# Kernel optimization log

Hardware: AMD Instinct MI355X
Metric: run time of the kernel (lower is better)

Reference implementation:

```python
import jax, jax.numpy as jnp
import numpy as np

KSIZE = 7
SIGMA = 3.0
ALPHA = 0.1
POS_VAL_FOR_ALL_NEG = 5.0
NEG_VAL_FOR_ALL_POS = -5.0


def _gauss_kernel():
    x = jnp.arange(KSIZE, dtype=jnp.float32) - (KSIZE - 1) / 2.0
    pdf = jnp.exp(-0.5 * (x / SIGMA) ** 2)
    return pdf / pdf.sum()


def _gaussian_blur(img):
    # img: (B, C, H, W); separable 7x7 gaussian, reflect padding (torchvision behavior)
    B, C, H, W = img.shape
    k = _gauss_kernel()
    pad = KSIZE // 2
    x = jnp.pad(img, ((0, 0), (0, 0), (pad, pad), (pad, pad)), mode='reflect')
    x = x.reshape(B * C, 1, H + 2 * pad, W + 2 * pad)
    kh = k.reshape(1, 1, KSIZE, 1)
    kw = k.reshape(1, 1, 1, KSIZE)
    x = jax.lax.conv_general_dilated(x, kh, (1, 1), 'VALID')
    x = jax.lax.conv_general_dilated(x, kw, (1, 1), 'VALID')
    return x.reshape(B, C, H, W)


def _dup_map(x, mask, fallback):
    # x, mask: (L,). Gather x[mask] (original order) then tile to length L.
    # Stable argsort puts True(=selected) positions first in original order.
    L = x.shape[0]
    cnt = mask.sum()
    order = jnp.argsort(jnp.logical_not(mask))  # selected indices first, stable
    idx = order[jnp.arange(L) % jnp.maximum(cnt, 1)]
    return jnp.where(cnt == 0, jnp.float32(fallback), x[idx])


_dup_vmapped = jax.vmap(_dup_map, in_axes=(0, 0, None))


def _bce_with_logits(x, y):
    # mean( max(x,0) - x*y + log1p(exp(-|x|)) ) == mean( softplus(x) - x*y )
    return jnp.mean(jnp.logaddexp(0.0, x) - x * y)


def _forward(inp, tgt):
    B, C, H, W = inp.shape
    aug_sim_target = (_gaussian_blur(tgt * 255.0) > 0).astype(jnp.float32)

    L = H * W
    x = inp.reshape(B * C, L)
    t = tgt.reshape(B * C, L)
    a = aug_sim_target.reshape(B * C, L)

    # duplicated_pos: gather input at target>0, tile; fallback +5 if no positives
    pos_mask = t > 0
    dup_pos = _dup_vmapped(x, pos_mask, POS_VAL_FOR_ALL_NEG)

    # duplicated_false_pos: prefer (input>0 & ~aug_pos); else all negatives; else -5
    aug_pos = a > 0
    fp_mask = jnp.logical_and(x > 0, jnp.logical_not(aug_pos))
    neg_mask = jnp.logical_not(aug_pos)
    cnt_fp = fp_mask.sum(axis=1, keepdims=True)
    chosen_mask = jnp.where(cnt_fp > 0, fp_mask, neg_mask)
    dup_fp = _dup_vmapped(x, chosen_mask, NEG_VAL_FOR_ALL_POS)

    sim = dup_pos * x
    aug_sim = dup_pos * dup_fp

    sim_loss = _bce_with_logits(sim, t) + _bce_with_logits(dup_pos, jnp.ones_like(x))
    aug_sim_loss = _bce_with_logits(aug_sim, jnp.zeros_like(x))
    return sim_loss + ALPHA * aug_sim_loss


def setup_inputs() -> dict:
    key = jax.random.key(0)
    k1, k2 = jax.random.split(key)
    B, C, H, W = 16, 3, 512, 512
    inp = jax.random.normal(k1, (B, C, H, W), dtype=jnp.float32)
    tgt = jax.random.randint(k2, (B, C, H, W), 0, 2).astype(jnp.float32)
    return {"input": inp, "target": tgt}


def reference(input, target):
    return _forward(input, target)
```

## Files before the change

### kernel.cpp

```cpp
#include <hip/hip_runtime.h>
#include <math.h>

constexpr int W = 512;
constexpr int HIMG = 512;
constexpr int L = 1 << 18;
constexpr int LOG2L = 18;
constexpr int TPB = 256;
constexpr int TILE = 2048;
constexpr int TILES_PER_ROW = L / TILE;
constexpr int WORDS_PER_ROW = L / 64;
constexpr int WORDS_PER_TILE = TILE / 64;
constexpr int LBLK = 32;
constexpr int CHUNK = L / LBLK;
constexpr int LIT = CHUNK / (TPB * 4);

typedef unsigned long long ull;

__device__ __forceinline__ float softplus_f(float v) {
    return fmaxf(v, 0.0f) +
           0.6931471805599453f *
               __builtin_amdgcn_logf(1.0f + __builtin_amdgcn_exp2f(-fabsf(v) * 1.4426950408889634f));
}

__device__ __forceinline__ ull hdil7(ull prev, ull cur, ull next) {
    ull r = cur;
    r |= (cur >> 1) | (next << 63);
    r |= (cur >> 2) | (next << 62);
    r |= (cur >> 3) | (next << 61);
    r |= (cur << 1) | (prev >> 63);
    r |= (cur << 2) | (prev >> 62);
    r |= (cur << 3) | (prev >> 61);
    return r;
}

template <typename T>
__device__ __forceinline__ T sel8(const T* a, int k) {
    return k == 0 ? a[0] : k == 1 ? a[1] : k == 2 ? a[2] : k == 3 ? a[3]
         : k == 4 ? a[4] : k == 5 ? a[5] : k == 6 ? a[6] : a[7];
}

__global__ void mask_dilh_kernel(const float* __restrict__ x, const float* __restrict__ t,
                                 ull* __restrict__ maskT, ull* __restrict__ maskX,
                                 ull* __restrict__ maskH, float* __restrict__ out,
                                 int nScan) {
    if (blockIdx.x == 0 && threadIdx.x == 0) out[0] = 0.0f;
    int lane = threadIdx.x & 63;
    int wave = (blockIdx.x * TPB + threadIdx.x) >> 6;
    int nW = (gridDim.x * TPB) >> 6;
    for (int s = wave; s < nScan; s += nW) {
        int eb = s << 9;
        ull wt[8], wx[8], h[8];
#pragma unroll
        for (int k = 0; k < 8; ++k) {
            wt[k] = __ballot(t[eb + k * 64 + lane] > 0.0f);
            wx[k] = __ballot(x[eb + k * 64 + lane] > 0.0f);
        }
#pragma unroll
        for (int k = 0; k < 8; ++k) {
            ull cur = wt[k];
            ull prev = k ? wt[k - 1]
                         : ((((cur >> 1) & 1ull) << 63) | (((cur >> 2) & 1ull) << 62) |
                            (((cur >> 3) & 1ull) << 61));
            ull next = (k < 7) ? wt[k + 1]
                               : (((cur >> 62) & 1ull) | (((cur >> 61) & 1ull) << 1) |
                                  (((cur >> 60) & 1ull) << 2));
            h[k] = hdil7(prev, cur, next);
        }
        int w0 = s << 3;
        int k = lane & 7;
        if (lane < 8) maskT[w0 + k] = sel8(wt, k);
        else if (lane < 16) maskX[w0 + k] = sel8(wx, k);
        else if (lane < 24) maskH[w0 + k] = sel8(h, k);
    }
}

__global__ __launch_bounds__(TPB)
void dilv_count_kernel(const ull* __restrict__ maskT, const ull* __restrict__ maskX,
                       const ull* __restrict__ maskH, ull* __restrict__ maskA,
                       int* __restrict__ oPos, int* __restrict__ oCh,
                       int* __restrict__ rCp, int* __restrict__ rCc,
                       ull* __restrict__ rMp, ull* __restrict__ rMc,
                       int* __restrict__ rUseFp) {
    int r = blockIdx.x;
    int tid = threadIdx.x;
    __shared__ ull sh[WORDS_PER_ROW];
    __shared__ unsigned char pw[WORDS_PER_ROW], fw[WORDS_PER_ROW], nw[WORDS_PER_ROW];
    int base = r * WORDS_PER_ROW;
#pragma unroll
    for (int c = 0; c < WORDS_PER_ROW / TPB; ++c) {
        int w = c * TPB + tid;
        sh[w] = maskH[base + w];
    }
    __syncthreads();
#pragma unroll
    for (int c = 0; c < WORDS_PER_ROW / TPB; ++c) {
        int w = c * TPB + tid;
        int scan = w >> 3, col = w & 7;
        ull wa = 0;
#pragma unroll
        for (int d = -3; d <= 3; ++d) {
            int ii = scan + d;
            ii = ii < 0 ? -ii : (ii > HIMG - 1 ? 2 * (HIMG - 1) - ii : ii);
            wa |= sh[ii * 8 + col];
        }
        maskA[base + w] = wa;
        ull wt = maskT[base + w], wx = maskX[base + w];
        pw[w] = (unsigned char)__popcll(wt);
        fw[w] = (unsigned char)__popcll(wx & ~wa);
        nw[w] = (unsigned char)(64 - __popcll(wa));
    }
    __syncthreads();
    __shared__ int ssp[TILES_PER_ROW], ssf[TILES_PER_ROW], ssn[TILES_PER_ROW];
    int myp = 0, myf = 0, myn = 0;
    if (tid < TILES_PER_ROW) {
        int wb = tid * WORDS_PER_TILE;
#pragma unroll 8
        for (int k = 0; k < WORDS_PER_TILE; ++k) {
            myp += pw[wb + k]; myf += fw[wb + k]; myn += nw[wb + k];
        }
        ssp[tid] = myp; ssf[tid] = myf; ssn[tid] = myn;
    }
    __syncthreads();
    for (int off = 1; off < TILES_PER_ROW; off <<= 1) {
        int ap = 0, af = 0, an = 0;
        bool act = (tid < TILES_PER_ROW && tid >= off);
        if (act) { ap = ssp[tid - off]; af = ssf[tid - off]; an = ssn[tid - off]; }
        __syncthreads();
        if (act) { ssp[tid] += ap; ssf[tid] += af; ssn[tid] += an; }
        __syncthreads();
    }
    if (tid < TILES_PER_ROW) {
        int cp = ssp[TILES_PER_ROW - 1], cf = ssf[TILES_PER_ROW - 1], cn = ssn[TILES_PER_ROW - 1];
        bool useFp = cf > 0;
        int tile = r * TILES_PER_ROW + tid;
        oPos[tile] = ssp[tid] - myp;
        oCh[tile] = useFp ? (ssf[tid] - myf) : (ssn[tid] - myn);
        if (tid == 0) {
            int cc = useFp ? cf : cn;
            rCp[r] = cp; rCc[r] = cc; rUseFp[r] = useFp ? 1 : 0;
            ull dp_ = (ull)(cp > 0 ? cp : 1);
            ull dc_ = (ull)(cc > 0 ? cc : 1);
            rMp[r] = ((1ull << 40) + dp_ - 1) / dp_;
            rMc[r] = ((1ull << 40) + dc_ - 1) / dc_;
        }
    }
}

__global__ void scatter_kernel(const float* __restrict__ x,
                               const ull* __restrict__ maskT, const ull* __restrict__ maskX,
                               const ull* __restrict__ maskA,
                               const int* __restrict__ oPos, const int* __restrict__ oCh,
                               const int* __restrict__ rUseFp,
                               float* __restrict__ xp, float* __restrict__ xf) {
    int tile = blockIdx.x;
    int tid = threadIdx.x;
    int r = tile >> 7;
    bool useFp = rUseFp[r] != 0;
    int widx = tile * WORDS_PER_TILE + (tid >> 3);
    int shift = (tid & 7) * 8;
    ull wa = maskA[widx];
    unsigned bT = (unsigned)(maskT[widx] >> shift) & 0xFF;
    unsigned bCh = useFp ? ((unsigned)((maskX[widx] & ~wa) >> shift) & 0xFF)
                         : ((unsigned)((~wa) >> shift) & 0xFF);
    const float4* x4 = (const float4*)x;
    int b4 = tile * (TILE / 4) + tid * 2;
    float4 a = x4[b4], b = x4[b4 + 1];
    float xv[8] = {a.x, a.y, a.z, a.w, b.x, b.y, b.z, b.w};
    int p = __popc(bT), c = __popc(bCh);
    __shared__ int s[TPB];
    int v = p | (c << 16);
    s[tid] = v;
    __syncthreads();
    for (int off = 1; off < TPB; off <<= 1) {
        int add = tid >= off ? s[tid - off] : 0;
        __syncthreads();
        s[tid] += add;
        __syncthreads();
    }
    int excl = s[tid] - v;
    int rL = r << LOG2L;
    int pwi = rL + oPos[tile] + (excl & 0xFFFF);
    int cwi = rL + oCh[tile] + (excl >> 16);
#pragma unroll
    for (int e = 0; e < 8; ++e) {
        if ((bT >> e) & 1) xp[pwi++] = xv[e];
        if ((bCh >> e) & 1) xf[cwi++] = xv[e];
    }
}

__global__ __launch_bounds__(TPB)
void loss_kernel(const float* __restrict__ x, const ull* __restrict__ maskT,
                 const float* __restrict__ xp, const float* __restrict__ xf,
                 const int* __restrict__ rCp, const int* __restrict__ rCc,
                 const ull* __restrict__ rMp, const ull* __restrict__ rMc,
                 float* __restrict__ out, double inv_ntot) {
    int r = blockIdx.x >> 5;
    int cb = (blockIdx.x & 31) * CHUNK;
    int rL = r << LOG2L;
    int cp = rCp[r], cc = rCc[r];
    ull Mp = rMp[r], Mc = rMc[r];
    const float4* x4 = (const float4*)(x + rL + cb);
    const float* xpr = xp + rL;
    const float* xfr = xf + rL;
    const ull* mtr = maskT + (rL >> 6);
    float local = 0.0f;
#pragma unroll
    for (int it = 0; it < LIT; ++it) {
        int o4 = it * TPB + threadIdx.x;
        unsigned l = (unsigned)(cb + (o4 << 2));
        float4 xv = x4[o4];
        unsigned tb = (unsigned)(mtr[l >> 6] >> (l & 63)) & 0xFu;
        float dps[4], dfs[4];
        if (cp > 0) {
            unsigned d = (unsigned)cp;
            unsigned q = (unsigned)(((ull)l * Mp) >> 40);
            unsigned m0 = l - q * d;
            unsigned m1 = m0 + 1; if (m1 == d) m1 = 0;
            unsigned m2 = m1 + 1; if (m2 == d) m2 = 0;
            unsigned m3 = m2 + 1; if (m3 == d) m3 = 0;
            dps[0] = xpr[m0]; dps[1] = xpr[m1]; dps[2] = xpr[m2]; dps[3] = xpr[m3];
        } else {
            dps[0] = dps[1] = dps[2] = dps[3] = 5.0f;
        }
        if (cc > 0) {
            unsigned d = (unsigned)cc;
            unsigned q = (unsigned)(((ull)l * Mc) >> 40);
            unsigned m0 = l - q * d;
            unsigned m1 = m0 + 1; if (m1 == d) m1 = 0;
            unsigned m2 = m1 + 1; if (m2 == d) m2 = 0;
            unsigned m3 = m2 + 1; if (m3 == d) m3 = 0;
            dfs[0] = xfr[m0]; dfs[1] = xfr[m1]; dfs[2] = xfr[m2]; dfs[3] = xfr[m3];
        } else {
            dfs[0] = dfs[1] = dfs[2] = dfs[3] = -5.0f;
        }
        float xs[4] = {xv.x, xv.y, xv.z, xv.w};
#pragma unroll
        for (int k = 0; k < 4; ++k) {
            float sim = dps[k] * xs[k];
            float e = softplus_f(sim) + softplus_f(-dps[k]) + 0.1f * softplus_f(dps[k] * dfs[k]);
            if ((tb >> k) & 1) e -= sim;
            local += e;
        }
    }
    __shared__ double sd[TPB];
    int tid = threadIdx.x;
    sd[tid] = (double)local;
    __syncthreads();
    for (int off = TPB / 2; off > 0; off >>= 1) {
        if (tid < off) sd[tid] += sd[tid + off];
        __syncthreads();
    }
    if (tid == 0) atomicAdd(out, (float)(sd[0] * inv_ntot));
}

extern "C" void kernel_launch(void* const* d_in, const int* in_sizes, int n_in,
                              void* d_out, int out_size, void* d_ws, size_t ws_size,
                              hipStream_t stream) {
    const float* x = (const float*)d_in[0];
    const float* t = (const float*)d_in[1];
    float* out = (float*)d_out;

    int ntot = in_sizes[0];
    int R = ntot >> LOG2L;
    int numTiles = ntot / TILE;
    int nwords = ntot / 64;
    int nScan = ntot / W;

    char* ws = (char*)d_ws;
    size_t off = 0;
    auto alloc = [&](size_t bytes) {
        size_t p = off;
        off = (off + bytes + 255) & ~(size_t)255;
        return (void*)(ws + p);
    };
    ull* maskT = (ull*)alloc((size_t)nwords * 8);
    ull* maskX = (ull*)alloc((size_t)nwords * 8);
    ull* maskH = (ull*)alloc((size_t)nwords * 8);
    ull* maskA = (ull*)alloc((size_t)nwords * 8);
    int* oPos = (int*)alloc(numTiles * sizeof(int));
    int* oCh  = (int*)alloc(numTiles * sizeof(int));
    int* rCp = (int*)alloc(R * sizeof(int));
    int* rCc = (int*)alloc(R * sizeof(int));
    int* rUseFp = (int*)alloc(R * sizeof(int));
    ull* rMp = (ull*)alloc(R * sizeof(ull));
    ull* rMc = (ull*)alloc(R * sizeof(ull));
    float* xp = (float*)alloc((size_t)ntot * sizeof(float));
    float* xf = (float*)alloc((size_t)ntot * sizeof(float));

    mask_dilh_kernel<<<1536, TPB, 0, stream>>>(x, t, maskT, maskX, maskH, out, nScan);
    dilv_count_kernel<<<R, TPB, 0, stream>>>(maskT, maskX, maskH, maskA, oPos, oCh,
                                             rCp, rCc, rMp, rMc, rUseFp);
    scatter_kernel<<<numTiles, TPB, 0, stream>>>(x, maskT, maskX, maskA, oPos, oCh, rUseFp,
                                                 xp, xf);
    loss_kernel<<<R * LBLK, TPB, 0, stream>>>(x, maskT, xp, xf, rCp, rCc, rMp, rMc, out,
                                              1.0 / (double)ntot);
}
```

Before: 176.1 us.

## Fuse horizontal and vertical dilation with per-tile counting; coalesce scatter via LDS staging

Merges the mask/horizontal-dilation kernel and the vertical-dilation/count kernel into one kernel. Each block handles 32 scanlines plus a 3-row halo in shared memory and emits the false-positive and negative masks along with per-tile counts through wave shuffles. A small scan kernel then computes the row offsets. The scatter kernel now stages compacted values in LDS and writes them out contiguously, replacing per-thread scattered stores. The cost is recomputing the halo rows of the target ballots and extra LDS use in scatter.

```diff
diff --git a/kernel.cpp b/kernel.cpp
--- a/kernel.cpp
+++ b/kernel.cpp
@@ -8,8 +8,11 @@
 constexpr int TPB = 256;
 constexpr int TILE = 2048;
 constexpr int TILES_PER_ROW = L / TILE;
-constexpr int WORDS_PER_ROW = L / 64;
 constexpr int WORDS_PER_TILE = TILE / 64;
+constexpr int SPB = 32;
+constexpr int HALO = 3;
+constexpr int HBUF = SPB + 2 * HALO;
+constexpr int BLK_PER_IMG = HIMG / SPB;
 constexpr int LBLK = 32;
 constexpr int CHUNK = L / LBLK;
 constexpr int LIT = CHUNK / (TPB * 4);
@@ -39,21 +42,35 @@
          : k == 4 ? a[4] : k == 5 ? a[5] : k == 6 ? a[6] : a[7];
 }
 
-__global__ void mask_dilh_kernel(const float* __restrict__ x, const float* __restrict__ t,
-                                 ull* __restrict__ maskT, ull* __restrict__ maskX,
-                                 ull* __restrict__ maskH, float* __restrict__ out,
-                                 int nScan) {
+__global__ __launch_bounds__(TPB)
+void fused_mask_kernel(const float* __restrict__ x, const float* __restrict__ t,
+                       ull* __restrict__ mT, ull* __restrict__ mFp, ull* __restrict__ mNeg,
+                       int* __restrict__ cPos, int* __restrict__ cFp, int* __restrict__ cNeg,
+                       float* __restrict__ out) {
     if (blockIdx.x == 0 && threadIdx.x == 0) out[0] = 0.0f;
+    int b = blockIdx.x;
+    int img = b >> 4;
+    int y0 = (b & 15) * SPB;
+    int gs0 = img * HIMG + y0;
+
+    __shared__ ull hbuf[HBUF][8];
+    __shared__ ull tbuf[SPB][8];
+    __shared__ ull xbuf[SPB][8];
+
     int lane = threadIdx.x & 63;
-    int wave = (blockIdx.x * TPB + threadIdx.x) >> 6;
-    int nW = (gridDim.x * TPB) >> 6;
-    for (int s = wave; s < nScan; s += nW) {
-        int eb = s << 9;
+    int wv = threadIdx.x >> 6;
+    int ylo = (y0 - HALO < 0) ? 0 : y0 - HALO;
+    int yhi = (y0 + SPB - 1 + HALO > HIMG - 1) ? HIMG - 1 : y0 + SPB - 1 + HALO;
+
+    for (int yl = ylo + wv; yl <= yhi; yl += 4) {
+        int gbase = (img * HIMG + yl) * W;
+        bool own = (yl >= y0) && (yl < y0 + SPB);
         ull wt[8], wx[8], h[8];
 #pragma unroll
-        for (int k = 0; k < 8; ++k) {
-            wt[k] = __ballot(t[eb + k * 64 + lane] > 0.0f);
-            wx[k] = __ballot(x[eb + k * 64 + lane] > 0.0f);
+        for (int k = 0; k < 8; ++k) wt[k] = __ballot(t[gbase + k * 64 + lane] > 0.0f);
+        if (own) {
+#pragma unroll
+            for (int k = 0; k < 8; ++k) wx[k] = __ballot(x[gbase + k * 64 + lane] > 0.0f);
         }
 #pragma unroll
         for (int k = 0; k < 8; ++k) {
@@ -66,108 +83,107 @@
                                   (((cur >> 60) & 1ull) << 2));
             h[k] = hdil7(prev, cur, next);
         }
-        int w0 = s << 3;
+        int hy = yl - (y0 - HALO);
         int k = lane & 7;
-        if (lane < 8) maskT[w0 + k] = sel8(wt, k);
-        else if (lane < 16) maskX[w0 + k] = sel8(wx, k);
-        else if (lane < 24) maskH[w0 + k] = sel8(h, k);
-    }
-}
-
-__global__ __launch_bounds__(TPB)
-void dilv_count_kernel(const ull* __restrict__ maskT, const ull* __restrict__ maskX,
-                       const ull* __restrict__ maskH, ull* __restrict__ maskA,
-                       int* __restrict__ oPos, int* __restrict__ oCh,
-                       int* __restrict__ rCp, int* __restrict__ rCc,
-                       ull* __restrict__ rMp, ull* __restrict__ rMc,
-                       int* __restrict__ rUseFp) {
+        if (lane < 8) {
+            hbuf[hy][k] = sel8(h, k);
+        } else if (own && lane < 16) {
+            tbuf[yl - y0][k] = sel8(wt, k);
+            mT[(img * HIMG + yl) * 8 + k] = sel8(wt, k);
+        } else if (own && lane < 24) {
+            xbuf[yl - y0][k] = sel8(wx, k);
+        }
+    }
+    __syncthreads();
+
+    int tid = threadIdx.x;
+    int ys = tid >> 3;
+    int c = tid & 7;
+    int y = y0 + ys;
+    ull wa = 0;
+#pragma unroll
+    for (int d = -3; d <= 3; ++d) {
+        int yy = y + d;
+        yy = yy < 0 ? -yy : (yy > HIMG - 1 ? 2 * (HIMG - 1) - yy : yy);
+        wa |= hbuf[yy - (y0 - HALO)][c];
+    }
+    ull tw = tbuf[ys][c];
+    ull fp = xbuf[ys][c] & ~wa;
+    ull ng = ~wa;
+    int gw = gs0 * 8 + tid;
+    mFp[gw] = fp;
+    mNeg[gw] = ng;
+    int pT = __popcll(tw), pF = __popcll(fp), pN = __popcll(ng);
+#pragma unroll
+    for (int m = 1; m < 32; m <<= 1) {
+        pT += __shfl_xor(pT, m, 64);
+        pF += __shfl_xor(pF, m, 64);
+        pN += __shfl_xor(pN, m, 64);
+    }
+    if ((lane & 31) == 0) {
+        int tile = img * TILES_PER_ROW + (y0 >> 2) + (tid >> 5);
+        cPos[tile] = pT; cFp[tile] = pF; cNeg[tile] = pN;
+    }
+}
+
+__global__ void scan_kernel(const int* __restrict__ cPos, const int* __restrict__ cFp,
+                            const int* __restrict__ cNeg,
+                            int* __restrict__ oPos, int* __restrict__ oCh,
+                            int* __restrict__ rCp, int* __restrict__ rCc,
+                            ull* __restrict__ rMp, ull* __restrict__ rMc,
+                            int* __restrict__ rUseFp) {
     int r = blockIdx.x;
     int tid = threadIdx.x;
-    __shared__ ull sh[WORDS_PER_ROW];
-    __shared__ unsigned char pw[WORDS_PER_ROW], fw[WORDS_PER_ROW], nw[WORDS_PER_ROW];
-    int base = r * WORDS_PER_ROW;
-#pragma unroll
-    for (int c = 0; c < WORDS_PER_ROW / TPB; ++c) {
-        int w = c * TPB + tid;
-        sh[w] = maskH[base + w];
-    }
-    __syncthreads();
-#pragma unroll
-    for (int c = 0; c < WORDS_PER_ROW / TPB; ++c) {
-        int w = c * TPB + tid;
-        int scan = w >> 3, col = w & 7;
-        ull wa = 0;
-#pragma unroll
-        for (int d = -3; d <= 3; ++d) {
-            int ii = scan + d;
-            ii = ii < 0 ? -ii : (ii > HIMG - 1 ? 2 * (HIMG - 1) - ii : ii);
-            wa |= sh[ii * 8 + col];
-        }
-        maskA[base + w] = wa;
-        ull wt = maskT[base + w], wx = maskX[base + w];
-        pw[w] = (unsigned char)__popcll(wt);
-        fw[w] = (unsigned char)__popcll(wx & ~wa);
-        nw[w] = (unsigned char)(64 - __popcll(wa));
-    }
-    __syncthreads();
     __shared__ int ssp[TILES_PER_ROW], ssf[TILES_PER_ROW], ssn[TILES_PER_ROW];
-    int myp = 0, myf = 0, myn = 0;
-    if (tid < TILES_PER_ROW) {
-        int wb = tid * WORDS_PER_TILE;
-#pragma unroll 8
-        for (int k = 0; k < WORDS_PER_TILE; ++k) {
-            myp += pw[wb + k]; myf += fw[wb + k]; myn += nw[wb + k];
-        }
-        ssp[tid] = myp; ssf[tid] = myf; ssn[tid] = myn;
-    }
+    int myp = cPos[r * TILES_PER_ROW + tid];
+    int myf = cFp[r * TILES_PER_ROW + tid];
+    int myn = cNeg[r * TILES_PER_ROW + tid];
+    ssp[tid] = myp; ssf[tid] = myf; ssn[tid] = myn;
     __syncthreads();
     for (int off = 1; off < TILES_PER_ROW; off <<= 1) {
         int ap = 0, af = 0, an = 0;
-        bool act = (tid < TILES_PER_ROW && tid >= off);
-        if (act) { ap = ssp[tid - off]; af = ssf[tid - off]; an = ssn[tid - off]; }
-        __syncthreads();
-        if (act) { ssp[tid] += ap; ssf[tid] += af; ssn[tid] += an; }
-        __syncthreads();
-    }
-    if (tid < TILES_PER_ROW) {
-        int cp = ssp[TILES_PER_ROW - 1], cf = ssf[TILES_PER_ROW - 1], cn = ssn[TILES_PER_ROW - 1];
-        bool useFp = cf > 0;
-        int tile = r * TILES_PER_ROW + tid;
-        oPos[tile] = ssp[tid] - myp;
-        oCh[tile] = useFp ? (ssf[tid] - myf) : (ssn[tid] - myn);
-        if (tid == 0) {
-            int cc = useFp ? cf : cn;
-            rCp[r] = cp; rCc[r] = cc; rUseFp[r] = useFp ? 1 : 0;
-            ull dp_ = (ull)(cp > 0 ? cp : 1);
-            ull dc_ = (ull)(cc > 0 ? cc : 1);
-            rMp[r] = ((1ull << 40) + dp_ - 1) / dp_;
-            rMc[r] = ((1ull << 40) + dc_ - 1) / dc_;
-        }
-    }
-}
-
-__global__ void scatter_kernel(const float* __restrict__ x,
-                               const ull* __restrict__ maskT, const ull* __restrict__ maskX,
-                               const ull* __restrict__ maskA,
-                               const int* __restrict__ oPos, const int* __restrict__ oCh,
-                               const int* __restrict__ rUseFp,
-                               float* __restrict__ xp, float* __restrict__ xf) {
+        if (tid >= off) { ap = ssp[tid - off]; af = ssf[tid - off]; an = ssn[tid - off]; }
+        __syncthreads();
+        if (tid >= off) { ssp[tid] += ap; ssf[tid] += af; ssn[tid] += an; }
+        __syncthreads();
+    }
+    int cp = ssp[TILES_PER_ROW - 1], cf = ssf[TILES_PER_ROW - 1], cn = ssn[TILES_PER_ROW - 1];
+    bool useFp = cf > 0;
+    int tile = r * TILES_PER_ROW + tid;
+    oPos[tile] = ssp[tid] - myp;
+    oCh[tile] = useFp ? (ssf[tid] - myf) : (ssn[tid] - myn);
+    if (tid == 0) {
+        int cc = useFp ? cf : cn;
+        rCp[r] = cp; rCc[r] = cc; rUseFp[r] = useFp ? 1 : 0;
+        ull dp_ = (ull)(cp > 0 ? cp : 1);
+        ull dc_ = (ull)(cc > 0 ? cc : 1);
+        rMp[r] = ((1ull << 40) + dp_ - 1) / dp_;
+        rMc[r] = ((1ull << 40) + dc_ - 1) / dc_;
+    }
+}
+
+__global__ __launch_bounds__(TPB)
+void scatter_kernel(const float* __restrict__ x, const ull* __restrict__ mT,
+                    const ull* __restrict__ mFp, const ull* __restrict__ mNeg,
+                    const int* __restrict__ oPos, const int* __restrict__ oCh,
+                    const int* __restrict__ rUseFp,
+                    float* __restrict__ xp, float* __restrict__ xf) {
     int tile = blockIdx.x;
     int tid = threadIdx.x;
     int r = tile >> 7;
     bool useFp = rUseFp[r] != 0;
     int widx = tile * WORDS_PER_TILE + (tid >> 3);
     int shift = (tid & 7) * 8;
-    ull wa = maskA[widx];
-    unsigned bT = (unsigned)(maskT[widx] >> shift) & 0xFF;
-    unsigned bCh = useFp ? ((unsigned)((maskX[widx] & ~wa) >> shift) & 0xFF)
-                         : ((unsigned)((~wa) >> shift) & 0xFF);
+    unsigned bT = (unsigned)(mT[widx] >> shift) & 0xFF;
+    ull chw = useFp ? mFp[widx] : mNeg[widx];
+    unsigned bCh = (unsigned)(chw >> shift) & 0xFF;
     const float4* x4 = (const float4*)x;
     int b4 = tile * (TILE / 4) + tid * 2;
     float4 a = x4[b4], b = x4[b4 + 1];
     float xv[8] = {a.x, a.y, a.z, a.w, b.x, b.y, b.z, b.w};
     int p = __popc(bT), c = __popc(bCh);
     __shared__ int s[TPB];
+    __shared__ float bufP[TILE], bufC[TILE];
     int v = p | (c << 16);
     s[tid] = v;
     __syncthreads();
@@ -178,18 +194,25 @@
         __syncthreads();
     }
     int excl = s[tid] - v;
+    int ep = excl & 0xFFFF;
+    int ec = excl >> 16;
+#pragma unroll
+    for (int e = 0; e < 8; ++e) {
+        if ((bT >> e) & 1) bufP[ep++] = xv[e];
+        if ((bCh >> e) & 1) bufC[ec++] = xv[e];
+    }
+    __syncthreads();
+    int tot = s[TPB - 1];
+    int P = tot & 0xFFFF, C = tot >> 16;
     int rL = r << LOG2L;
-    int pwi = rL + oPos[tile] + (excl & 0xFFFF);
-    int cwi = rL + oCh[tile] + (excl >> 16);
-#pragma unroll
-    for (int e = 0; e < 8; ++e) {
-        if ((bT >> e) & 1) xp[pwi++] = xv[e];
-        if ((bCh >> e) & 1) xf[cwi++] = xv[e];
-    }
+    int pbase = rL + oPos[tile];
+    for (int i = tid; i < P; i += TPB) xp[pbase + i] = bufP[i];
+    int cbase = rL + oCh[tile];
+    for (int i = tid; i < C; i += TPB) xf[cbase + i] = bufC[i];
 }
 
 __global__ __launch_bounds__(TPB)
-void loss_kernel(const float* __restrict__ x, const ull* __restrict__ maskT,
+void loss_kernel(const float* __restrict__ x, const ull* __restrict__ mT,
                  const float* __restrict__ xp, const float* __restrict__ xf,
                  const int* __restrict__ rCp, const int* __restrict__ rCc,
                  const ull* __restrict__ rMp, const ull* __restrict__ rMc,
@@ -202,7 +225,7 @@
     const float4* x4 = (const float4*)(x + rL + cb);
     const float* xpr = xp + rL;
     const float* xfr = xf + rL;
-    const ull* mtr = maskT + (rL >> 6);
+    const ull* mtr = mT + (rL >> 6);
     float local = 0.0f;
 #pragma unroll
     for (int it = 0; it < LIT; ++it) {
@@ -264,7 +287,7 @@
     int R = ntot >> LOG2L;
     int numTiles = ntot / TILE;
     int nwords = ntot / 64;
-    int nScan = ntot / W;
+    int nMaskBlk = ntot / (SPB * W);
 
     char* ws = (char*)d_ws;
     size_t off = 0;
@@ -273,10 +296,12 @@
         off = (off + bytes + 255) & ~(size_t)255;
         return (void*)(ws + p);
     };
-    ull* maskT = (ull*)alloc((size_t)nwords * 8);
-    ull* maskX = (ull*)alloc((size_t)nwords * 8);
-    ull* maskH = (ull*)alloc((size_t)nwords * 8);
-    ull* maskA = (ull*)alloc((size_t)nwords * 8);
+    ull* mT   = (ull*)alloc((size_t)nwords * 8);
+    ull* mFp  = (ull*)alloc((size_t)nwords * 8);
+    ull* mNeg = (ull*)alloc((size_t)nwords * 8);
+    int* cPos = (int*)alloc(numTiles * sizeof(int));
+    int* cFp  = (int*)alloc(numTiles * sizeof(int));
+    int* cNeg = (int*)alloc(numTiles * sizeof(int));
     int* oPos = (int*)alloc(numTiles * sizeof(int));
     int* oCh  = (int*)alloc(numTiles * sizeof(int));
     int* rCp = (int*)alloc(R * sizeof(int));
@@ -287,11 +312,10 @@
     float* xp = (float*)alloc((size_t)ntot * sizeof(float));
     float* xf = (float*)alloc((size_t)ntot * sizeof(float));
 
-    mask_dilh_kernel<<<1536, TPB, 0, stream>>>(x, t, maskT, maskX, maskH, out, nScan);
-    dilv_count_kernel<<<R, TPB, 0, stream>>>(maskT, maskX, maskH, maskA, oPos, oCh,
-                                             rCp, rCc, rMp, rMc, rUseFp);
-    scatter_kernel<<<numTiles, TPB, 0, stream>>>(x, maskT, maskX, maskA, oPos, oCh, rUseFp,
-                                                 xp, xf);
-    loss_kernel<<<R * LBLK, TPB, 0, stream>>>(x, maskT, xp, xf, rCp, rCc, rMp, rMc, out,
+    fused_mask_kernel<<<nMaskBlk, TPB, 0, stream>>>(x, t, mT, mFp, mNeg, cPos, cFp, cNeg, out);
+    scan_kernel<<<R, TILES_PER_ROW, 0, stream>>>(cPos, cFp, cNeg, oPos, oCh,
+                                                 rCp, rCc, rMp, rMc, rUseFp);
+    scatter_kernel<<<numTiles, TPB, 0, stream>>>(x, mT, mFp, mNeg, oPos, oCh, rUseFp, xp, xf);
+    loss_kernel<<<R * LBLK, TPB, 0, stream>>>(x, mT, xp, xf, rCp, rCc, rMp, rMc, out,
                                               1.0 / (double)ntot);
 }
```

Measured after the change: 171.6 us. 1.03x faster.
